# Kernel tuning notes

Measured on AMD Instinct MI355X. Metric: run time of the kernel, lower is better.

Reference implementation:

```python
import jax, jax.numpy as jnp
import numpy as np

B, N, D, L, E = 16, 256, 128, 3, 32768  # graphs, nodes/graph, hidden_dim, num_layers, edges


def _ln(x, g, b, eps=1e-5):
    mu = jnp.mean(x, -1, keepdims=True)
    xc = x - mu
    var = jnp.mean(xc * xc, -1, keepdims=True)
    return xc * jax.lax.rsqrt(var + eps) * g + b


def setup_inputs() -> dict:
    key = jax.random.key(0)
    ks = jax.random.split(key, 16)

    def w(k, shape, fan):
        return jax.random.normal(k, shape, jnp.float32) * (fan ** -0.5)

    x = jax.random.normal(ks[0], (B * N, 1), jnp.float32)
    batch = (jnp.arange(B * N) // N).astype(jnp.int32)
    # E//B edges per graph, endpoints local to that graph (global ids = g*N + local)
    eb = jnp.repeat(jnp.arange(B, dtype=jnp.int32), E // B)
    src = jax.random.randint(ks[1], (E,), 0, N, dtype=jnp.int32)
    dst = jax.random.randint(ks[2], (E,), 0, N, dtype=jnp.int32)
    edge_index = jnp.stack([eb * N + src, eb * N + dst])
    edge_attr = jax.random.normal(ks[3], (E, 1), jnp.float32) * 0.5

    return {
        "x": x,
        "edge_index": edge_index,
        "edge_attr": edge_attr,
        "batch": batch,
        "enc_W": w(ks[4], (1, D), 1),
        "enc_b": jnp.zeros((D,), jnp.float32),
        "msg_W": w(ks[5], (L, 2 * D + 1, D), 2 * D + 1),
        "msg_b": jnp.zeros((L, D), jnp.float32),
        "msg_g": jnp.ones((L, D), jnp.float32),
        "msg_beta": jnp.zeros((L, D), jnp.float32),
        "upd_W": w(ks[6], (L, 2 * D, D), 2 * D),
        "upd_b": jnp.zeros((L, D), jnp.float32),
        "upd_g": jnp.ones((L, D), jnp.float32),
        "upd_beta": jnp.zeros((L, D), jnp.float32),
        "dec_W1": w(ks[7], (2 * D + 1, D), 2 * D + 1),
        "dec_b1": jnp.zeros((D,), jnp.float32),
        "dec_W2": w(ks[8], (D, D // 2), D),
        "dec_b2": jnp.zeros((D // 2,), jnp.float32),
        "dec_W3": w(ks[9], (D // 2, 1), D // 2),
        "dec_b3": jnp.zeros((1,), jnp.float32),
    }


def reference(x, edge_index, edge_attr, batch, enc_W, enc_b,
              msg_W, msg_b, msg_g, msg_beta,
              upd_W, upd_b, upd_g, upd_beta,
              dec_W1, dec_b1, dec_W2, dec_b2, dec_W3, dec_b3):
    n = N
    b = x.shape[0] // n
    # node encoder then dense batch: (B, N, D)
    h = (x @ enc_W + enc_b).reshape(b, n, D)

    src = edge_index[0] % n
    dst = edge_index[1] % n
    eb = batch[edge_index[0]]
    # to_dense_adj (scatter-add duplicates) then symmetrize
    adj = jnp.zeros((b, n, n), h.dtype).at[eb, src, dst].add(edge_attr[:, 0])
    adj = adj + jnp.swapaxes(adj, 1, 2)

    mask = (1.0 - jnp.eye(n, dtype=h.dtype))[None, :, :, None]  # zero self-messages
    for l in range(L):
        # cat([h_target(i), h_source(j), J]) @ W decomposed to avoid the 2D+1 concat
        Wt, Ws, wj = msg_W[l, :D], msg_W[l, D:2 * D], msg_W[l, 2 * D]
        pre = (h @ Wt)[:, :, None, :] + (h @ Ws)[:, None, :, :] \
              + adj[..., None] * wj + msg_b[l]          # (B, N, N, D)
        msgs = jax.nn.silu(_ln(pre, msg_g[l], msg_beta[l]))
        agg = jnp.sum(msgs * mask, axis=2)               # (B, N, D)
        u = jnp.concatenate([h, agg], -1) @ upd_W[l] + upd_b[l]
        h = h + jax.nn.silu(_ln(u, upd_g[l], upd_beta[l]))

    h_src = h[eb, src]
    h_dst = h[eb, dst]
    e = jnp.concatenate([h_src, h_dst, edge_attr], -1)
    e = jax.nn.silu(e @ dec_W1 + dec_b1)
    e = jax.nn.silu(e @ dec_W2 + dec_b2)
    out = jnp.tanh(e @ dec_W3 + dec_b3)
    return out[:, 0]
```

## Files before the change

kernel.cpp:

```cpp
#include <hip/hip_runtime.h>

#define NB 16
#define NN 256
#define DD 128
#define NL 3
#define NE 32768
#define BN 4096

__device__ __forceinline__ float siluf(float y) {
  return __fdividef(y, 1.0f + __expf(-y));
}

template<int CTRL>
__device__ __forceinline__ float dpp_add(float x) {
  int v = __builtin_amdgcn_update_dpp(0, __float_as_int(x), CTRL, 0xF, 0xF, true);
  return x + __int_as_float(v);
}

__device__ __forceinline__ float sum16(float x) {
  x = dpp_add<0xB1>(x);
  x = dpp_add<0x4E>(x);
  x = dpp_add<0x141>(x);
  x = dpp_add<0x140>(x);
  return x;
}

__device__ __forceinline__ float sum32(float x) {
  x = sum16(x);
  int v = __builtin_amdgcn_ds_swizzle(__float_as_int(x), 0x401F);
  return x + __int_as_float(v);
}

__device__ __forceinline__ float sum64(float x) {
  x = sum32(x);
  return x + __shfl_xor(x, 32, 64);
}


__global__ __launch_bounds__(256) void k_encode(
    const float* __restrict__ x, const float* __restrict__ W,
    const float* __restrict__ bb, float* __restrict__ h) {
  int t = blockIdx.x * 256 + threadIdx.x;
  int i = t >> 5;
  int c = (t & 31) << 2;
  float xv = x[i];
  float4 w = *(const float4*)(W + c);
  float4 bv = *(const float4*)(bb + c);
  float4 o;
  o.x = fmaf(xv, w.x, bv.x); o.y = fmaf(xv, w.y, bv.y);
  o.z = fmaf(xv, w.z, bv.z); o.w = fmaf(xv, w.w, bv.w);
  *(float4*)(h + i * DD + c) = o;
}

__global__ __launch_bounds__(256) void k_scatter(
    const int* __restrict__ ei, const float* __restrict__ ea,
    float* __restrict__ adj) {
  int e = blockIdx.x * 256 + threadIdx.x;
  int g0 = ei[e];
  int g1 = ei[NE + e];
  float v = ea[e];
  int b = g0 >> 8;
  int s = g0 & 255;
  int d = g1 & 255;
  atomicAdd(adj + (b * NN + s) * NN + d, v);
  atomicAdd(adj + (b * NN + d) * NN + s, v);
}

__global__ __launch_bounds__(64) void k_wprep(
    const float* __restrict__ msgW, float* __restrict__ wst) {
  int l = blockIdx.x;
  const float* wj = msgW + (size_t)l * (2 * DD + 1) * DD + 2 * DD * DD;
  int d0 = threadIdx.x << 1;
  float2 wv = *(const float2*)(wj + d0);
  float s1 = sum64(wv.x + wv.y);
  float s2 = sum64(fmaf(wv.x, wv.x, wv.y * wv.y));
  if (threadIdx.x == 0)
    *(float2*)(wst + 2 * l) = make_float2(s1 * 0.0078125f, s2 * 0.0078125f);
}

__global__ __launch_bounds__(256) void k_gemm2(
    const float* __restrict__ A, const float* __restrict__ W1,
    const float* __restrict__ W2, const float* __restrict__ bias1,
    const float* __restrict__ wj,
    float* __restrict__ C1, float* __restrict__ C2,
    float* __restrict__ statT, float* __restrict__ statS) {
  __shared__ float sa[8][128];
  int r = threadIdx.x >> 5;
  int c4 = (threadIdx.x & 31) << 2;
  int row0 = blockIdx.x << 3;
  ((float4*)&sa[0][0])[threadIdx.x] = ((const float4*)(A + row0 * DD))[threadIdx.x];
  __syncthreads();
  float4 a1 = {0.f, 0.f, 0.f, 0.f}, a2 = {0.f, 0.f, 0.f, 0.f};
  #pragma unroll 4
  for (int m = 0; m < DD; ++m) {
    float a = sa[r][m];
    float4 w1 = *(const float4*)(W1 + m * DD + c4);
    float4 w2 = *(const float4*)(W2 + m * DD + c4);
    a1.x = fmaf(a, w1.x, a1.x); a1.y = fmaf(a, w1.y, a1.y);
    a1.z = fmaf(a, w1.z, a1.z); a1.w = fmaf(a, w1.w, a1.w);
    a2.x = fmaf(a, w2.x, a2.x); a2.y = fmaf(a, w2.y, a2.y);
    a2.z = fmaf(a, w2.z, a2.z); a2.w = fmaf(a, w2.w, a2.w);
  }
  if (bias1) {
    float4 bv = *(const float4*)(bias1 + c4);
    a1.x += bv.x; a1.y += bv.y; a1.z += bv.z; a1.w += bv.w;
  }
  int rw = row0 + r;
  *(float4*)(C1 + rw * DD + c4) = a1;
  *(float4*)(C2 + rw * DD + c4) = a2;
  if (wj) {
    float4 wv = *(const float4*)(wj + c4);
    float s1t = sum32((a1.x + a1.y) + (a1.z + a1.w));
    float s2t = sum32(fmaf(a1.x, a1.x, a1.y * a1.y) + fmaf(a1.z, a1.z, a1.w * a1.w));
    float s3t = sum32(fmaf(a1.x, wv.x, a1.y * wv.y) + fmaf(a1.z, wv.z, a1.w * wv.w));
    float s1s = sum32((a2.x + a2.y) + (a2.z + a2.w));
    float s2s = sum32(fmaf(a2.x, a2.x, a2.y * a2.y) + fmaf(a2.z, a2.z, a2.w * a2.w));
    float s3s = sum32(fmaf(a2.x, wv.x, a2.y * wv.y) + fmaf(a2.z, wv.z, a2.w * wv.w));
    if ((threadIdx.x & 31) == 0) {
      const float inv = 0.0078125f;
      ((float4*)statT)[rw] = make_float4(s1t * inv, s2t * inv, s3t * inv, 0.f);
      ((float4*)statS)[rw] = make_float4(s1s * inv, s2s * inv, s3s * inv, 0.f);
    }
  }
}

__global__ __launch_bounds__(256) void k_ts(
    const float* __restrict__ T, const float* __restrict__ S,
    const float* __restrict__ adj,
    const float* __restrict__ statT, const float* __restrict__ statS,
    const float* __restrict__ wst, float* __restrict__ MR4) {
  __shared__ float sT[64][64];
  __shared__ float sS[64][64];
  int b = blockIdx.x >> 4;
  int i0 = ((blockIdx.x >> 2) & 3) << 6;
  int j0 = (blockIdx.x & 3) << 6;
  int t = threadIdx.x;
  int ti = t >> 4, tj = t & 15;
  float acc[4][4] = {};
  int sr = t >> 2, scg = t & 3;
  const float* Trow = T + ((size_t)(b * NN + i0 + sr)) * DD + scg * 16;
  const float* Srow = S + ((size_t)(b * NN + j0 + sr)) * DD + scg * 16;
  for (int kc = 0; kc < 2; ++kc) {
    __syncthreads();
    #pragma unroll
    for (int m = 0; m < 4; ++m) {
      float4 v = *(const float4*)(Trow + kc * 64 + m * 4);
      int kk = scg * 16 + m * 4;
      sT[kk + 0][sr] = v.x; sT[kk + 1][sr] = v.y;
      sT[kk + 2][sr] = v.z; sT[kk + 3][sr] = v.w;
      float4 u = *(const float4*)(Srow + kc * 64 + m * 4);
      sS[kk + 0][sr] = u.x; sS[kk + 1][sr] = u.y;
      sS[kk + 2][sr] = u.z; sS[kk + 3][sr] = u.w;
    }
    __syncthreads();
    #pragma unroll 4
    for (int k = 0; k < 64; ++k) {
      float4 rt = *(const float4*)&sT[k][ti << 2];
      float4 rs = *(const float4*)&sS[k][tj << 2];
      acc[0][0] = fmaf(rt.x, rs.x, acc[0][0]);
      acc[0][1] = fmaf(rt.x, rs.y, acc[0][1]);
      acc[0][2] = fmaf(rt.x, rs.z, acc[0][2]);
      acc[0][3] = fmaf(rt.x, rs.w, acc[0][3]);
      acc[1][0] = fmaf(rt.y, rs.x, acc[1][0]);
      acc[1][1] = fmaf(rt.y, rs.y, acc[1][1]);
      acc[1][2] = fmaf(rt.y, rs.z, acc[1][2]);
      acc[1][3] = fmaf(rt.y, rs.w, acc[1][3]);
      acc[2][0] = fmaf(rt.z, rs.x, acc[2][0]);
      acc[2][1] = fmaf(rt.z, rs.y, acc[2][1]);
      acc[2][2] = fmaf(rt.z, rs.z, acc[2][2]);
      acc[2][3] = fmaf(rt.z, rs.w, acc[2][3]);
      acc[3][0] = fmaf(rt.w, rs.x, acc[3][0]);
      acc[3][1] = fmaf(rt.w, rs.y, acc[3][1]);
      acc[3][2] = fmaf(rt.w, rs.z, acc[3][2]);
      acc[3][3] = fmaf(rt.w, rs.w, acc[3][3]);
    }
  }
  float2 ws = *(const float2*)wst;
  float4 stT[4], stS[4];
  #pragma unroll
  for (int o = 0; o < 4; ++o) {
    stT[o] = ((const float4*)statT)[b * NN + i0 + (ti << 2) + o];
    stS[o] = ((const float4*)statS)[b * NN + j0 + (tj << 2) + o];
  }
  #pragma unroll
  for (int oi = 0; oi < 4; ++oi) {
    int row = b * NN + i0 + (ti << 2) + oi;
    float4 av = *(const float4*)(adj + (size_t)row * NN + j0 + (tj << 2));
    float4* m4row = (float4*)MR4 + (size_t)row * NN + j0 + (tj << 2);
    #pragma unroll
    for (int oj = 0; oj < 4; ++oj) {
      float a = (oj == 0) ? av.x : (oj == 1) ? av.y : (oj == 2) ? av.z : av.w;
      float mean = stT[oi].x + stS[oj].x + a * ws.x;
      float e2 = stT[oi].y + stS[oj].y + a * a * ws.y
               + fmaf(acc[oi][oj], 0.015625f, 2.f * a * (stT[oi].z + stS[oj].z));
      float var = fmaf(-mean, mean, e2);
      float Rv = rsqrtf(var + 1e-5f);
      m4row[oj] = make_float4(Rv, -mean * Rv, a, 0.f);
    }
  }
}

__global__ __launch_bounds__(512, 6) void k_messages(
    const float* __restrict__ hT, const float* __restrict__ hS,
    const float* __restrict__ MR4, const float* __restrict__ wj,
    const float* __restrict__ mg, const float* __restrict__ mbe,
    float* __restrict__ agg) {
  __shared__ float sh[64 * 128];
  __shared__ float4 smr[256];
  const float LN2 = 0.6931471805599453f;
  const float L2E = 1.4426950408889634f;
  int b = blockIdx.x >> 6;
  int i0 = (blockIdx.x & 63) << 2;
  int t = threadIdx.x;
  int w = t >> 6, lane = t & 63;
  int il = w >> 1, jh = w & 1, jb = jh << 5;
  int i = i0 + il, row = b * NN + i;
  int d0 = lane << 1;
  float2 tv = *(const float2*)(hT + (size_t)row * DD + d0);
  float2 wv = *(const float2*)(wj + d0);
  float2 gv = *(const float2*)(mg + d0);
  float2 bev = *(const float2*)(mbe + d0);
  float G0 = gv.x * L2E, G1 = gv.y * L2E;
  float BE0 = bev.x * L2E, BE1 = bev.y * L2E;
  float acc0 = 0.f, acc1 = 0.f;

  const float4* hsrc = (const float4*)(hS + (size_t)(b * NN) * DD);
  int ml = t >> 6, mj = t & 63;
  const float4* msrc = (const float4*)MR4 + (size_t)(b * NN + i0 + ml) * NN + mj;

  float4 p0 = hsrc[t], p1 = hsrc[t + 512], p2 = hsrc[t + 1024], p3 = hsrc[t + 1536];
  float4 pm;
  if (t < 256) pm = msrc[0];
  ((float4*)sh)[t] = p0; ((float4*)sh)[t + 512] = p1;
  ((float4*)sh)[t + 1024] = p2; ((float4*)sh)[t + 1536] = p3;
  if (t < 256) smr[t] = pm;
  __syncthreads();

  const float4* mrw = smr + (il << 6) + jb;

  for (int c = 0; c < 4; ++c) {
    if (c < 3) {
      const float4* hn = hsrc + (c + 1) * 2048;
      p0 = hn[t]; p1 = hn[t + 512]; p2 = hn[t + 1024]; p3 = hn[t + 1536];
      if (t < 256) pm = msrc[(c + 1) * 64];
    }
    #pragma unroll 4
    for (int jj = 0; jj < 32; ++jj) {
      float4 m4 = mrw[jj];
      float2 hs = *(const float2*)(sh + ((jb + jj) << 7) + d0);
      float v0 = tv.x + hs.x; v0 = fmaf(m4.z, wv.x, v0);
      float v1 = tv.y + hs.y; v1 = fmaf(m4.z, wv.y, v1);
      float z0 = fmaf(m4.x, v0, m4.y);
      float z1 = fmaf(m4.x, v1, m4.y);
      float yl0 = fmaf(G0, z0, BE0);
      float yl1 = fmaf(G1, z1, BE1);
      float e0 = __builtin_amdgcn_exp2f(-yl0);
      float e1 = __builtin_amdgcn_exp2f(-yl1);
      float den0 = 1.0f + e0, den1 = 1.0f + e1;
      float r = __builtin_amdgcn_rcpf(den0 * den1);
      acc0 = fmaf(yl0 * den1, r, acc0);
      acc1 = fmaf(yl1 * den0, r, acc1);
    }
    if ((i >> 6) == c && ((i >> 5) & 1) == jh) {
      int li = i & 31;
      float4 m4 = mrw[li];
      float2 hs = *(const float2*)(sh + ((jb + li) << 7) + d0);
      float v0 = tv.x + hs.x; v0 = fmaf(m4.z, wv.x, v0);
      float v1 = tv.y + hs.y; v1 = fmaf(m4.z, wv.y, v1);
      float z0 = fmaf(m4.x, v0, m4.y);
      float z1 = fmaf(m4.x, v1, m4.y);
      float yl0 = fmaf(G0, z0, BE0);
      float yl1 = fmaf(G1, z1, BE1);
      float e0 = __builtin_amdgcn_exp2f(-yl0);
      float e1 = __builtin_amdgcn_exp2f(-yl1);
      float den0 = 1.0f + e0, den1 = 1.0f + e1;
      float r = __builtin_amdgcn_rcpf(den0 * den1);
      acc0 = fmaf(yl0 * den1, -r, acc0);
      acc1 = fmaf(yl1 * den0, -r, acc1);
    }
    __syncthreads();
    if (c < 3) {
      ((float4*)sh)[t] = p0; ((float4*)sh)[t + 512] = p1;
      ((float4*)sh)[t + 1024] = p2; ((float4*)sh)[t + 1536] = p3;
      if (t < 256) smr[t] = pm;
      __syncthreads();
    }
  }
  if (jh == 1)
    ((float2*)smr)[(il << 6) + lane] = make_float2(acc0, acc1);
  __syncthreads();
  if (jh == 0) {
    float2 o = ((float2*)smr)[(il << 6) + lane];
    acc0 += o.x; acc1 += o.y;
    *(float2*)(agg + (size_t)row * DD + d0) =
        make_float2(acc0 * LN2, acc1 * LN2);
  }
}

__global__ __launch_bounds__(256) void k_update(
    float* __restrict__ h, const float* __restrict__ agg,
    const float* __restrict__ W, const float* __restrict__ ub,
    const float* __restrict__ ug, const float* __restrict__ ube) {
  __shared__ float scat[8][256];
  int r = threadIdx.x >> 5;
  int c4 = (threadIdx.x & 31) << 2;
  int row0 = blockIdx.x << 3;
  {
    int t = threadIdx.x;
    float4 v = ((const float4*)(h + row0 * DD))[t];
    int f = t << 2; int rr = f >> 7; int mm = f & 127;
    *(float4*)&scat[rr][mm] = v;
    float4 va = ((const float4*)(agg + row0 * DD))[t];
    *(float4*)&scat[rr][DD + mm] = va;
  }
  __syncthreads();
  float4 acc = *(const float4*)(ub + c4);
  #pragma unroll 4
  for (int m = 0; m < 2 * DD; ++m) {
    float a = scat[r][m];
    float4 wv = *(const float4*)(W + m * DD + c4);
    acc.x = fmaf(a, wv.x, acc.x);
    acc.y = fmaf(a, wv.y, acc.y);
    acc.z = fmaf(a, wv.z, acc.z);
    acc.w = fmaf(a, wv.w, acc.w);
  }
  float s1 = sum32((acc.x + acc.y) + (acc.z + acc.w));
  float s2 = sum32(fmaf(acc.x, acc.x, acc.y * acc.y) + fmaf(acc.z, acc.z, acc.w * acc.w));
  float mean = s1 * 0.0078125f;
  float var = fmaf(-mean, mean, s2 * 0.0078125f);
  float rstd = rsqrtf(var + 1e-5f);
  float4 g  = *(const float4*)(ug + c4);
  float4 be = *(const float4*)(ube + c4);
  float4 ho = *(const float4*)&scat[r][c4];
  float4 o;
  o.x = ho.x + siluf(fmaf((acc.x - mean) * rstd, g.x, be.x));
  o.y = ho.y + siluf(fmaf((acc.y - mean) * rstd, g.y, be.y));
  o.z = ho.z + siluf(fmaf((acc.z - mean) * rstd, g.z, be.z));
  o.w = ho.w + siluf(fmaf((acc.w - mean) * rstd, g.w, be.w));
  *(float4*)(h + (row0 + r) * DD + c4) = o;
}

__global__ __launch_bounds__(256, 2) void k_decoder(
    const int* __restrict__ ei, const float* __restrict__ ea,
    const float* __restrict__ P, const float* __restrict__ Q,
    const float* __restrict__ w1e, const float* __restrict__ b1,
    const float* __restrict__ W2, const float* __restrict__ b2,
    const float* __restrict__ W3, const float* __restrict__ b3,
    float* __restrict__ out) {
  __shared__ float sS[64][132];
  int t = threadIdx.x;
  {
    int e = t >> 2, qq = t & 3;
    int eg = (blockIdx.x << 6) + e;
    int g0 = ei[eg], g1 = ei[NE + eg];
    float av = ea[eg];
    const float4* p4 = (const float4*)(P + (size_t)g0 * DD + qq * 32);
    const float4* q4 = (const float4*)(Q + (size_t)g1 * DD + qq * 32);
    const float4* w4 = (const float4*)(w1e + qq * 32);
    const float4* b4 = (const float4*)(b1 + qq * 32);
    #pragma unroll
    for (int m = 0; m < 8; ++m) {
      float4 p = p4[m], qv = q4[m], wv = w4[m], bv = b4[m];
      float4 sv;
      sv.x = siluf(fmaf(av, wv.x, (p.x + qv.x) + bv.x));
      sv.y = siluf(fmaf(av, wv.y, (p.y + qv.y) + bv.y));
      sv.z = siluf(fmaf(av, wv.z, (p.z + qv.z) + bv.z));
      sv.w = siluf(fmaf(av, wv.w, (p.w + qv.w) + bv.w));
      *(float4*)&sS[e][(qq << 5) + (m << 2)] = sv;
    }
  }
  __syncthreads();
  int ti = t >> 4, tj = t & 15;
  float4 acc[4] = {{0.f,0.f,0.f,0.f},{0.f,0.f,0.f,0.f},{0.f,0.f,0.f,0.f},{0.f,0.f,0.f,0.f}};
  const float4* W2g = (const float4*)W2;
  #pragma unroll 4
  for (int k4 = 0; k4 < 32; ++k4) {
    float4 sv[4], wv[4];
    #pragma unroll
    for (int r = 0; r < 4; ++r)
      sv[r] = *(const float4*)&sS[(ti << 2) + r][k4 << 2];
    #pragma unroll
    for (int kk = 0; kk < 4; ++kk)
      wv[kk] = W2g[(((k4 << 2) + kk) << 4) + tj];
    #pragma unroll
    for (int r = 0; r < 4; ++r) {
      acc[r].x = fmaf(sv[r].x, wv[0].x, acc[r].x);
      acc[r].y = fmaf(sv[r].x, wv[0].y, acc[r].y);
      acc[r].z = fmaf(sv[r].x, wv[0].z, acc[r].z);
      acc[r].w = fmaf(sv[r].x, wv[0].w, acc[r].w);
      acc[r].x = fmaf(sv[r].y, wv[1].x, acc[r].x);
      acc[r].y = fmaf(sv[r].y, wv[1].y, acc[r].y);
      acc[r].z = fmaf(sv[r].y, wv[1].z, acc[r].z);
      acc[r].w = fmaf(sv[r].y, wv[1].w, acc[r].w);
      acc[r].x = fmaf(sv[r].z, wv[2].x, acc[r].x);
      acc[r].y = fmaf(sv[r].z, wv[2].y, acc[r].y);
      acc[r].z = fmaf(sv[r].z, wv[2].z, acc[r].z);
      acc[r].w = fmaf(sv[r].z, wv[2].w, acc[r].w);
      acc[r].x = fmaf(sv[r].w, wv[3].x, acc[r].x);
      acc[r].y = fmaf(sv[r].w, wv[3].y, acc[r].y);
      acc[r].z = fmaf(sv[r].w, wv[3].z, acc[r].z);
      acc[r].w = fmaf(sv[r].w, wv[3].w, acc[r].w);
    }
  }
  float4 b2v = *(const float4*)(b2 + (tj << 2));
  float4 w3v = *(const float4*)(W3 + (tj << 2));
  float b3v = b3[0];
  #pragma unroll
  for (int r = 0; r < 4; ++r) {
    float part = siluf(acc[r].x + b2v.x) * w3v.x;
    part = fmaf(siluf(acc[r].y + b2v.y), w3v.y, part);
    part = fmaf(siluf(acc[r].z + b2v.z), w3v.z, part);
    part = fmaf(siluf(acc[r].w + b2v.w), w3v.w, part);
    part = sum16(part);
    if (tj == 0)
      out[(blockIdx.x << 6) + (ti << 2) + r] = tanhf(part + b3v);
  }
}

extern "C" void kernel_launch(void* const* d_in, const int* in_sizes, int n_in,
                              void* d_out, int out_size, void* d_ws, size_t ws_size,
                              hipStream_t stream) {
  const float* x     = (const float*)d_in[0];
  const int*   ei    = (const int*)  d_in[1];
  const float* ea    = (const float*)d_in[2];
  const float* encW  = (const float*)d_in[4];
  const float* encb  = (const float*)d_in[5];
  const float* msgW  = (const float*)d_in[6];
  const float* msgb  = (const float*)d_in[7];
  const float* msgg  = (const float*)d_in[8];
  const float* msgbe = (const float*)d_in[9];
  const float* updW  = (const float*)d_in[10];
  const float* updb  = (const float*)d_in[11];
  const float* updg  = (const float*)d_in[12];
  const float* updbe = (const float*)d_in[13];
  const float* dW1   = (const float*)d_in[14];
  const float* db1   = (const float*)d_in[15];
  const float* dW2   = (const float*)d_in[16];
  const float* db2   = (const float*)d_in[17];
  const float* dW3   = (const float*)d_in[18];
  const float* db3   = (const float*)d_in[19];
  float* out = (float*)d_out;

  float* h     = (float*)d_ws;
  float* adj   = h     + BN * DD;
  float* hT    = adj   + NB * NN * NN;
  float* hS    = hT    + BN * DD;
  float* agg   = hS    + BN * DD;
  float* statT = agg   + BN * DD;
  float* statS = statT + BN * 4;
  float* wst   = statS + BN * 4;
  float* MR4   = wst   + 8;

  hipMemsetAsync(adj, 0, (size_t)NB * NN * NN * sizeof(float), stream);
  k_encode<<<512, 256, 0, stream>>>(x, encW, encb, h);
  k_scatter<<<NE / 256, 256, 0, stream>>>(ei, ea, adj);
  k_wprep<<<NL, 64, 0, stream>>>(msgW, wst);

  for (int l = 0; l < NL; ++l) {
    const float* Wl = msgW + (size_t)l * (2 * DD + 1) * DD;
    const float* wjl = Wl + 2 * DD * DD;
    k_gemm2<<<BN / 8, 256, 0, stream>>>(h, Wl, Wl + DD * DD, msgb + l * DD, wjl,
                                        hT, hS, statT, statS);
    k_ts<<<256, 256, 0, stream>>>(hT, hS, adj, statT, statS, wst + 2 * l, MR4);
    k_messages<<<1024, 512, 0, stream>>>(hT, hS, MR4, wjl,
        msgg + l * DD, msgbe + l * DD, agg);
    k_update<<<BN / 8, 256, 0, stream>>>(h, agg, updW + (size_t)l * 2 * DD * DD,
        updb + l * DD, updg + l * DD, updbe + l * DD);
  }

  k_gemm2<<<BN / 8, 256, 0, stream>>>(h, dW1, dW1 + DD * DD, nullptr, nullptr,
                                      hT, hS, statT, statS);
  k_decoder<<<NE / 64, 256, 0, stream>>>(ei, ea, hT, hS, dW1 + 2 * DD * DD, db1,
      dW2, db2, dW3, db3, out);
}
```

Baseline: 327.2 us.

## Process two target rows per wave in k_messages and replace memset with zero kernel

Each wave in the message kernel now handles two target nodes over a quarter of the source range, so each shared-memory hS read is reused for two rows. The per-pair MR4 statistics are read straight from global memory through wave-uniform (readfirstlane) pointers instead of being staged in LDS. Partial sums are merged across four j-quarters through a small LDS buffer. Launch bounds drop from 6 to 4 waves per SIMD to give more registers. The adjacency memset is replaced by a custom zeroing kernel. The trade is lower occupancy and more scalar or global loads in exchange for fewer LDS reads per message.

```diff
diff --git a/kernel.cpp b/kernel.cpp
--- a/kernel.cpp
+++ b/kernel.cpp
@@ -36,6 +36,20 @@
   return x + __shfl_xor(x, 32, 64);
 }
 
+__device__ __forceinline__ const float4* uptr4(const float4* p) {
+  unsigned long long v = (unsigned long long)p;
+  unsigned lo = __builtin_amdgcn_readfirstlane((unsigned)v);
+  unsigned hi = __builtin_amdgcn_readfirstlane((unsigned)(v >> 32));
+  return (const float4*)(((unsigned long long)hi << 32) | (unsigned long long)lo);
+}
+
+
+__global__ __launch_bounds__(256) void k_zero(float4* __restrict__ p) {
+  int t = blockIdx.x * 256 + threadIdx.x;
+  float4 z = make_float4(0.f, 0.f, 0.f, 0.f);
+  p[t] = z;
+  p[t + 131072] = z;
+}
 
 __global__ __launch_bounds__(256) void k_encode(
     const float* __restrict__ x, const float* __restrict__ W,
@@ -200,56 +214,89 @@
   }
 }
 
-__global__ __launch_bounds__(512, 6) void k_messages(
+__global__ __launch_bounds__(512, 4) void k_messages(
     const float* __restrict__ hT, const float* __restrict__ hS,
     const float* __restrict__ MR4, const float* __restrict__ wj,
     const float* __restrict__ mg, const float* __restrict__ mbe,
     float* __restrict__ agg) {
   __shared__ float sh[64 * 128];
-  __shared__ float4 smr[256];
+  __shared__ float2 smerge[4][4][64];
   const float LN2 = 0.6931471805599453f;
   const float L2E = 1.4426950408889634f;
   int b = blockIdx.x >> 6;
   int i0 = (blockIdx.x & 63) << 2;
   int t = threadIdx.x;
   int w = t >> 6, lane = t & 63;
-  int il = w >> 1, jh = w & 1, jb = jh << 5;
-  int i = i0 + il, row = b * NN + i;
+  int ip = w >> 2;
+  int jq = w & 3;
+  int iA = i0 + (ip << 1), iB = iA + 1;
+  int rowA = b * NN + iA, rowB = b * NN + iB;
   int d0 = lane << 1;
-  float2 tv = *(const float2*)(hT + (size_t)row * DD + d0);
-  float2 wv = *(const float2*)(wj + d0);
-  float2 gv = *(const float2*)(mg + d0);
+  float2 tvA = *(const float2*)(hT + (size_t)rowA * DD + d0);
+  float2 tvB = *(const float2*)(hT + (size_t)rowB * DD + d0);
+  float2 wv  = *(const float2*)(wj + d0);
+  float2 gv  = *(const float2*)(mg + d0);
   float2 bev = *(const float2*)(mbe + d0);
   float G0 = gv.x * L2E, G1 = gv.y * L2E;
   float BE0 = bev.x * L2E, BE1 = bev.y * L2E;
-  float acc0 = 0.f, acc1 = 0.f;
-
+  float accA0 = 0.f, accA1 = 0.f, accB0 = 0.f, accB1 = 0.f;
+
+  const float4* mA = uptr4((const float4*)MR4 + (size_t)rowA * NN);
+  const float4* mB = uptr4((const float4*)MR4 + (size_t)rowB * NN);
   const float4* hsrc = (const float4*)(hS + (size_t)(b * NN) * DD);
-  int ml = t >> 6, mj = t & 63;
-  const float4* msrc = (const float4*)MR4 + (size_t)(b * NN + i0 + ml) * NN + mj;
 
   float4 p0 = hsrc[t], p1 = hsrc[t + 512], p2 = hsrc[t + 1024], p3 = hsrc[t + 1536];
-  float4 pm;
-  if (t < 256) pm = msrc[0];
   ((float4*)sh)[t] = p0; ((float4*)sh)[t + 512] = p1;
   ((float4*)sh)[t + 1024] = p2; ((float4*)sh)[t + 1536] = p3;
-  if (t < 256) smr[t] = pm;
   __syncthreads();
 
-  const float4* mrw = smr + (il << 6) + jb;
+  int jb = jq << 4;
 
   for (int c = 0; c < 4; ++c) {
     if (c < 3) {
       const float4* hn = hsrc + (c + 1) * 2048;
       p0 = hn[t]; p1 = hn[t + 512]; p2 = hn[t + 1024]; p3 = hn[t + 1536];
-      if (t < 256) pm = msrc[(c + 1) * 64];
     }
     #pragma unroll 4
-    for (int jj = 0; jj < 32; ++jj) {
-      float4 m4 = mrw[jj];
+    for (int jj = 0; jj < 16; ++jj) {
+      int j = (c << 6) + jb + jj;
+      float4 m4A = mA[j];
+      float4 m4B = mB[j];
       float2 hs = *(const float2*)(sh + ((jb + jj) << 7) + d0);
-      float v0 = tv.x + hs.x; v0 = fmaf(m4.z, wv.x, v0);
-      float v1 = tv.y + hs.y; v1 = fmaf(m4.z, wv.y, v1);
+      {
+        float v0 = fmaf(m4A.z, wv.x, tvA.x + hs.x);
+        float v1 = fmaf(m4A.z, wv.y, tvA.y + hs.y);
+        float z0 = fmaf(m4A.x, v0, m4A.y);
+        float z1 = fmaf(m4A.x, v1, m4A.y);
+        float yl0 = fmaf(G0, z0, BE0);
+        float yl1 = fmaf(G1, z1, BE1);
+        float e0 = __builtin_amdgcn_exp2f(-yl0);
+        float e1 = __builtin_amdgcn_exp2f(-yl1);
+        float den0 = 1.0f + e0, den1 = 1.0f + e1;
+        float r = __builtin_amdgcn_rcpf(den0 * den1);
+        accA0 = fmaf(yl0 * den1, r, accA0);
+        accA1 = fmaf(yl1 * den0, r, accA1);
+      }
+      {
+        float v0 = fmaf(m4B.z, wv.x, tvB.x + hs.x);
+        float v1 = fmaf(m4B.z, wv.y, tvB.y + hs.y);
+        float z0 = fmaf(m4B.x, v0, m4B.y);
+        float z1 = fmaf(m4B.x, v1, m4B.y);
+        float yl0 = fmaf(G0, z0, BE0);
+        float yl1 = fmaf(G1, z1, BE1);
+        float e0 = __builtin_amdgcn_exp2f(-yl0);
+        float e1 = __builtin_amdgcn_exp2f(-yl1);
+        float den0 = 1.0f + e0, den1 = 1.0f + e1;
+        float r = __builtin_amdgcn_rcpf(den0 * den1);
+        accB0 = fmaf(yl0 * den1, r, accB0);
+        accB1 = fmaf(yl1 * den0, r, accB1);
+      }
+    }
+    if ((iA >> 6) == c && ((iA >> 4) & 3) == jq) {
+      float4 m4 = mA[iA];
+      float2 hs = *(const float2*)(sh + ((iA & 63) << 7) + d0);
+      float v0 = fmaf(m4.z, wv.x, tvA.x + hs.x);
+      float v1 = fmaf(m4.z, wv.y, tvA.y + hs.y);
       float z0 = fmaf(m4.x, v0, m4.y);
       float z1 = fmaf(m4.x, v1, m4.y);
       float yl0 = fmaf(G0, z0, BE0);
@@ -258,15 +305,14 @@
       float e1 = __builtin_amdgcn_exp2f(-yl1);
       float den0 = 1.0f + e0, den1 = 1.0f + e1;
       float r = __builtin_amdgcn_rcpf(den0 * den1);
-      acc0 = fmaf(yl0 * den1, r, acc0);
-      acc1 = fmaf(yl1 * den0, r, acc1);
-    }
-    if ((i >> 6) == c && ((i >> 5) & 1) == jh) {
-      int li = i & 31;
-      float4 m4 = mrw[li];
-      float2 hs = *(const float2*)(sh + ((jb + li) << 7) + d0);
-      float v0 = tv.x + hs.x; v0 = fmaf(m4.z, wv.x, v0);
-      float v1 = tv.y + hs.y; v1 = fmaf(m4.z, wv.y, v1);
+      accA0 = fmaf(yl0 * den1, -r, accA0);
+      accA1 = fmaf(yl1 * den0, -r, accA1);
+    }
+    if ((iB >> 6) == c && ((iB >> 4) & 3) == jq) {
+      float4 m4 = mB[iB];
+      float2 hs = *(const float2*)(sh + ((iB & 63) << 7) + d0);
+      float v0 = fmaf(m4.z, wv.x, tvB.x + hs.x);
+      float v1 = fmaf(m4.z, wv.y, tvB.y + hs.y);
       float z0 = fmaf(m4.x, v0, m4.y);
       float z1 = fmaf(m4.x, v1, m4.y);
       float yl0 = fmaf(G0, z0, BE0);
@@ -275,25 +321,26 @@
       float e1 = __builtin_amdgcn_exp2f(-yl1);
       float den0 = 1.0f + e0, den1 = 1.0f + e1;
       float r = __builtin_amdgcn_rcpf(den0 * den1);
-      acc0 = fmaf(yl0 * den1, -r, acc0);
-      acc1 = fmaf(yl1 * den0, -r, acc1);
+      accB0 = fmaf(yl0 * den1, -r, accB0);
+      accB1 = fmaf(yl1 * den0, -r, accB1);
     }
     __syncthreads();
     if (c < 3) {
       ((float4*)sh)[t] = p0; ((float4*)sh)[t + 512] = p1;
       ((float4*)sh)[t + 1024] = p2; ((float4*)sh)[t + 1536] = p3;
-      if (t < 256) smr[t] = pm;
       __syncthreads();
     }
   }
-  if (jh == 1)
-    ((float2*)smr)[(il << 6) + lane] = make_float2(acc0, acc1);
+  smerge[(ip << 1) + 0][jq][lane] = make_float2(accA0, accA1);
+  smerge[(ip << 1) + 1][jq][lane] = make_float2(accB0, accB1);
   __syncthreads();
-  if (jh == 0) {
-    float2 o = ((float2*)smr)[(il << 6) + lane];
-    acc0 += o.x; acc1 += o.y;
-    *(float2*)(agg + (size_t)row * DD + d0) =
-        make_float2(acc0 * LN2, acc1 * LN2);
+  if (w < 4) {
+    float2 a0 = smerge[w][0][lane], a1 = smerge[w][1][lane];
+    float2 a2 = smerge[w][2][lane], a3 = smerge[w][3][lane];
+    float sx = (a0.x + a1.x) + (a2.x + a3.x);
+    float sy = (a0.y + a1.y) + (a2.y + a3.y);
+    *(float2*)(agg + (size_t)(b * NN + i0 + w) * DD + d0) =
+        make_float2(sx * LN2, sy * LN2);
   }
 }
 
@@ -451,7 +498,7 @@
   float* wst   = statS + BN * 4;
   float* MR4   = wst   + 8;
 
-  hipMemsetAsync(adj, 0, (size_t)NB * NN * NN * sizeof(float), stream);
+  k_zero<<<512, 256, 0, stream>>>((float4*)adj);
   k_encode<<<512, 256, 0, stream>>>(x, encW, encb, h);
   k_scatter<<<NE / 256, 256, 0, stream>>>(ei, ea, adj);
   k_wprep<<<NL, 64, 0, stream>>>(msgW, wst);
```

Result: slower. 360.1 us (+10.1%).

## Remap message kernel to 4-wide channels per lane and replace memset with zero kernel

Applied to the files above, without the earlier changes.

Changes the k_messages thread mapping so each lane handles four channels (float4) of a half-wave row, with each wave covering two target nodes and one quarter of the source nodes per chunk. All MR4 stats for the block's four rows are staged into shared memory once up front, and a four-way shared-memory reduction replaces the two-way one. Each shared hS load now feeds two target rows, which roughly halves LDS traffic per element and raises ILP, at the cost of more registers. The hipMemsetAsync of the adjacency buffer is replaced by a small custom zero kernel, which may cut API overhead.

```diff
diff --git a/kernel.cpp b/kernel.cpp
--- a/kernel.cpp
+++ b/kernel.cpp
@@ -36,6 +36,13 @@
   return x + __shfl_xor(x, 32, 64);
 }
 
+
+__global__ __launch_bounds__(256) void k_zero(float4* __restrict__ p) {
+  int t = blockIdx.x * 256 + threadIdx.x;
+  float4 z = make_float4(0.f, 0.f, 0.f, 0.f);
+  p[t] = z;
+  p[t + 131072] = z;
+}
 
 __global__ __launch_bounds__(256) void k_encode(
     const float* __restrict__ x, const float* __restrict__ W,
@@ -206,94 +213,127 @@
     const float* __restrict__ mg, const float* __restrict__ mbe,
     float* __restrict__ agg) {
   __shared__ float sh[64 * 128];
-  __shared__ float4 smr[256];
+  __shared__ float4 smr[4 * 256];
   const float LN2 = 0.6931471805599453f;
   const float L2E = 1.4426950408889634f;
   int b = blockIdx.x >> 6;
   int i0 = (blockIdx.x & 63) << 2;
   int t = threadIdx.x;
   int w = t >> 6, lane = t & 63;
-  int il = w >> 1, jh = w & 1, jb = jh << 5;
-  int i = i0 + il, row = b * NN + i;
-  int d0 = lane << 1;
-  float2 tv = *(const float2*)(hT + (size_t)row * DD + d0);
-  float2 wv = *(const float2*)(wj + d0);
-  float2 gv = *(const float2*)(mg + d0);
-  float2 bev = *(const float2*)(mbe + d0);
-  float G0 = gv.x * L2E, G1 = gv.y * L2E;
-  float BE0 = bev.x * L2E, BE1 = bev.y * L2E;
-  float acc0 = 0.f, acc1 = 0.f;
-
+  int p = w >> 2;
+  int q = w & 3;
+  int half = lane >> 5, li = lane & 31;
+  int iloc = (p << 1) + half;
+  int i = i0 + iloc;
+  int row = b * NN + i;
+  int d0 = li << 2;
+  float4 tv = *(const float4*)(hT + (size_t)row * DD + d0);
+  float4 wv = *(const float4*)(wj + d0);
+  float4 gv = *(const float4*)(mg + d0);
+  float4 be = *(const float4*)(mbe + d0);
+  float G0 = gv.x * L2E, G1 = gv.y * L2E, G2 = gv.z * L2E, G3 = gv.w * L2E;
+  float B0 = be.x * L2E, B1 = be.y * L2E, B2 = be.z * L2E, B3 = be.w * L2E;
+  float a0 = 0.f, a1 = 0.f, a2 = 0.f, a3 = 0.f;
+
+  {
+    const float4* msrc = (const float4*)MR4 + (size_t)(b * NN + i0) * NN;
+    smr[t] = msrc[t];
+    smr[t + 512] = msrc[t + 512];
+  }
   const float4* hsrc = (const float4*)(hS + (size_t)(b * NN) * DD);
-  int ml = t >> 6, mj = t & 63;
-  const float4* msrc = (const float4*)MR4 + (size_t)(b * NN + i0 + ml) * NN + mj;
-
   float4 p0 = hsrc[t], p1 = hsrc[t + 512], p2 = hsrc[t + 1024], p3 = hsrc[t + 1536];
-  float4 pm;
-  if (t < 256) pm = msrc[0];
   ((float4*)sh)[t] = p0; ((float4*)sh)[t + 512] = p1;
   ((float4*)sh)[t + 1024] = p2; ((float4*)sh)[t + 1536] = p3;
-  if (t < 256) smr[t] = pm;
   __syncthreads();
 
-  const float4* mrw = smr + (il << 6) + jb;
+  const float4* mbase = smr + (iloc << 8) + (q << 4);
+  const float* shbase = sh + ((q << 4) << 7) + d0;
 
   for (int c = 0; c < 4; ++c) {
     if (c < 3) {
       const float4* hn = hsrc + (c + 1) * 2048;
       p0 = hn[t]; p1 = hn[t + 512]; p2 = hn[t + 1024]; p3 = hn[t + 1536];
-      if (t < 256) pm = msrc[(c + 1) * 64];
-    }
+    }
+    const float4* mrow = mbase + (c << 6);
     #pragma unroll 4
-    for (int jj = 0; jj < 32; ++jj) {
-      float4 m4 = mrw[jj];
-      float2 hs = *(const float2*)(sh + ((jb + jj) << 7) + d0);
-      float v0 = tv.x + hs.x; v0 = fmaf(m4.z, wv.x, v0);
-      float v1 = tv.y + hs.y; v1 = fmaf(m4.z, wv.y, v1);
+    for (int jj = 0; jj < 16; ++jj) {
+      float4 m4 = mrow[jj];
+      float4 hs = *(const float4*)(shbase + (jj << 7));
+      float v0 = fmaf(m4.z, wv.x, tv.x + hs.x);
+      float v1 = fmaf(m4.z, wv.y, tv.y + hs.y);
+      float v2 = fmaf(m4.z, wv.z, tv.z + hs.z);
+      float v3 = fmaf(m4.z, wv.w, tv.w + hs.w);
       float z0 = fmaf(m4.x, v0, m4.y);
       float z1 = fmaf(m4.x, v1, m4.y);
-      float yl0 = fmaf(G0, z0, BE0);
-      float yl1 = fmaf(G1, z1, BE1);
-      float e0 = __builtin_amdgcn_exp2f(-yl0);
-      float e1 = __builtin_amdgcn_exp2f(-yl1);
-      float den0 = 1.0f + e0, den1 = 1.0f + e1;
-      float r = __builtin_amdgcn_rcpf(den0 * den1);
-      acc0 = fmaf(yl0 * den1, r, acc0);
-      acc1 = fmaf(yl1 * den0, r, acc1);
-    }
-    if ((i >> 6) == c && ((i >> 5) & 1) == jh) {
-      int li = i & 31;
-      float4 m4 = mrw[li];
-      float2 hs = *(const float2*)(sh + ((jb + li) << 7) + d0);
-      float v0 = tv.x + hs.x; v0 = fmaf(m4.z, wv.x, v0);
-      float v1 = tv.y + hs.y; v1 = fmaf(m4.z, wv.y, v1);
+      float z2 = fmaf(m4.x, v2, m4.y);
+      float z3 = fmaf(m4.x, v3, m4.y);
+      float y0 = fmaf(G0, z0, B0);
+      float y1 = fmaf(G1, z1, B1);
+      float y2 = fmaf(G2, z2, B2);
+      float y3 = fmaf(G3, z3, B3);
+      float e0 = __builtin_amdgcn_exp2f(-y0);
+      float e1 = __builtin_amdgcn_exp2f(-y1);
+      float e2 = __builtin_amdgcn_exp2f(-y2);
+      float e3 = __builtin_amdgcn_exp2f(-y3);
+      float d0v = 1.0f + e0, d1v = 1.0f + e1;
+      float d2v = 1.0f + e2, d3v = 1.0f + e3;
+      float r01 = __builtin_amdgcn_rcpf(d0v * d1v);
+      float r23 = __builtin_amdgcn_rcpf(d2v * d3v);
+      a0 = fmaf(y0 * d1v, r01, a0);
+      a1 = fmaf(y1 * d0v, r01, a1);
+      a2 = fmaf(y2 * d3v, r23, a2);
+      a3 = fmaf(y3 * d2v, r23, a3);
+    }
+    if (((i >> 6) == c) && (((i >> 4) & 3) == q)) {
+      float4 m4 = smr[(iloc << 8) + i];
+      float4 hs = *(const float4*)(sh + ((i & 63) << 7) + d0);
+      float v0 = fmaf(m4.z, wv.x, tv.x + hs.x);
+      float v1 = fmaf(m4.z, wv.y, tv.y + hs.y);
+      float v2 = fmaf(m4.z, wv.z, tv.z + hs.z);
+      float v3 = fmaf(m4.z, wv.w, tv.w + hs.w);
       float z0 = fmaf(m4.x, v0, m4.y);
       float z1 = fmaf(m4.x, v1, m4.y);
-      float yl0 = fmaf(G0, z0, BE0);
-      float yl1 = fmaf(G1, z1, BE1);
-      float e0 = __builtin_amdgcn_exp2f(-yl0);
-      float e1 = __builtin_amdgcn_exp2f(-yl1);
-      float den0 = 1.0f + e0, den1 = 1.0f + e1;
-      float r = __builtin_amdgcn_rcpf(den0 * den1);
-      acc0 = fmaf(yl0 * den1, -r, acc0);
-      acc1 = fmaf(yl1 * den0, -r, acc1);
+      float z2 = fmaf(m4.x, v2, m4.y);
+      float z3 = fmaf(m4.x, v3, m4.y);
+      float y0 = fmaf(G0, z0, B0);
+      float y1 = fmaf(G1, z1, B1);
+      float y2 = fmaf(G2, z2, B2);
+      float y3 = fmaf(G3, z3, B3);
+      float e0 = __builtin_amdgcn_exp2f(-y0);
+      float e1 = __builtin_amdgcn_exp2f(-y1);
+      float e2 = __builtin_amdgcn_exp2f(-y2);
+      float e3 = __builtin_amdgcn_exp2f(-y3);
+      float d0v = 1.0f + e0, d1v = 1.0f + e1;
+      float d2v = 1.0f + e2, d3v = 1.0f + e3;
+      float r01 = __builtin_amdgcn_rcpf(d0v * d1v);
+      float r23 = __builtin_amdgcn_rcpf(d2v * d3v);
+      a0 = fmaf(y0 * d1v, -r01, a0);
+      a1 = fmaf(y1 * d0v, -r01, a1);
+      a2 = fmaf(y2 * d3v, -r23, a2);
+      a3 = fmaf(y3 * d2v, -r23, a3);
     }
     __syncthreads();
     if (c < 3) {
       ((float4*)sh)[t] = p0; ((float4*)sh)[t + 512] = p1;
       ((float4*)sh)[t + 1024] = p2; ((float4*)sh)[t + 1536] = p3;
-      if (t < 256) smr[t] = pm;
       __syncthreads();
     }
   }
-  if (jh == 1)
-    ((float2*)smr)[(il << 6) + lane] = make_float2(acc0, acc1);
+  float4* smg = (float4*)sh;
+  smg[(((iloc << 2) + q) << 5) + li] = make_float4(a0, a1, a2, a3);
   __syncthreads();
-  if (jh == 0) {
-    float2 o = ((float2*)smr)[(il << 6) + lane];
-    acc0 += o.x; acc1 += o.y;
-    *(float2*)(agg + (size_t)row * DD + d0) =
-        make_float2(acc0 * LN2, acc1 * LN2);
+  if (t < 128) {
+    int il2 = t >> 5, l2 = t & 31;
+    float4 s0 = smg[(((il2 << 2) + 0) << 5) + l2];
+    float4 s1 = smg[(((il2 << 2) + 1) << 5) + l2];
+    float4 s2 = smg[(((il2 << 2) + 2) << 5) + l2];
+    float4 s3 = smg[(((il2 << 2) + 3) << 5) + l2];
+    float4 o;
+    o.x = ((s0.x + s1.x) + (s2.x + s3.x)) * LN2;
+    o.y = ((s0.y + s1.y) + (s2.y + s3.y)) * LN2;
+    o.z = ((s0.z + s1.z) + (s2.z + s3.z)) * LN2;
+    o.w = ((s0.w + s1.w) + (s2.w + s3.w)) * LN2;
+    *(float4*)(agg + (size_t)(b * NN + i0 + il2) * DD + (l2 << 2)) = o;
   }
 }
 
@@ -451,7 +491,7 @@
   float* wst   = statS + BN * 4;
   float* MR4   = wst   + 8;
 
-  hipMemsetAsync(adj, 0, (size_t)NB * NN * NN * sizeof(float), stream);
+  k_zero<<<512, 256, 0, stream>>>((float4*)adj);
   k_encode<<<512, 256, 0, stream>>>(x, encW, encb, h);
   k_scatter<<<NE / 256, 256, 0, stream>>>(ei, ea, adj);
   k_wprep<<<NL, 64, 0, stream>>>(msgW, wst);
```

Result: no change. 329.3 us (+0.6%).
